# Performance work log

Hardware: AMD Instinct MI355X
Metric: run time of the kernel (lower is better)

## Reference

```python
import jax, jax.numpy as jnp
import numpy as np


def _up2(x):
    return jnp.repeat(jnp.repeat(x, 2, axis=2), 2, axis=3)


def setup_inputs() -> dict:
    key = jax.random.key(0)
    ks = jax.random.split(key, 6)
    Vps, C, H, W = 32, 128, 64, 64
    return {
        "x1": jax.random.normal(ks[0], (Vps, C, H, W), dtype=jnp.float32),
        "x2": jax.random.normal(ks[1], (Vps, C, H // 2, W // 2), dtype=jnp.float32),
        "x3": jax.random.normal(ks[2], (Vps, C, H // 4, W // 4), dtype=jnp.float32),
        "x4": jax.random.normal(ks[3], (Vps, C, H // 4, W // 4), dtype=jnp.float32),
        "conv_w": jax.random.normal(ks[4], (128, 512), dtype=jnp.float32) * 0.02,
        "conv_b": jnp.zeros((128,), dtype=jnp.float32),
        "gamma": jnp.zeros((1,), dtype=jnp.float32),
        "weight": jnp.ones((128,), dtype=jnp.float32),
        "lin_w": jax.random.normal(ks[5], (1, 128), dtype=jnp.float32) * 0.1,
    }


def reference(x1, x2, x3, x4, conv_w, conv_b, gamma, weight, lin_w):
    # upsample lower pyramid levels to x1 resolution and concat on channels
    x_sm = jnp.concatenate([x1, _up2(x2), _up2(_up2(x3)), _up2(_up2(x4))], axis=1)
    # 1x1 conv: [Vps,512,H,W] x [128,512] -> [Vps,128,H,W]
    x_sm = jnp.einsum('vchw,oc->vohw', x_sm, conv_w) + conv_b[None, :, None, None]
    Vps, C, H, W = x_sm.shape

    # --- batch (viewport) attention ---
    gap = jnp.mean(x_sm, axis=(2, 3))                     # [Vps, C]
    v_q = gap @ lin_w.T                                    # [Vps, 1]
    att = v_q @ v_q.T                                      # [Vps, Vps]
    att_new = jnp.broadcast_to(jnp.max(att, axis=-1, keepdims=True), att.shape)
    vps_mat = jax.nn.softmax(att_new, axis=-1)             # rows constant -> uniform
    v_v = x_sm.reshape(Vps, C * H * W)
    vps_att = (vps_mat @ v_v).reshape(Vps, C, H, W)
    x_sm = vps_att * gamma + x_sm

    # --- channel attention ---
    c_q = jnp.mean(x_sm, axis=(2, 3))                      # [Vps, C]
    att_C = c_q.T @ c_q                                    # [C, C]
    C_mat = jax.nn.softmax(att_C, axis=-1) * weight        # broadcast over last dim
    c_v = x_sm.reshape(C, Vps * H * W)                     # faithful raw reshape as in torch
    C_att = (C_mat @ c_v).reshape(Vps, C, H, W)
    out = C_att + x_sm
    return out.reshape(Vps, C, H * W)
```

## Files before the change

### kernel.cpp

```cpp
#include <hip/hip_runtime.h>

#define V 32
#define CH 128
#define SP 4096

typedef __attribute__((ext_vector_type(8))) short bf16x8;
typedef __attribute__((ext_vector_type(4))) float f32x4;

__device__ __forceinline__ unsigned short bf16rne(float x) {
    union { float f; unsigned u; } v; v.f = x;
    unsigned r = v.u + 0x7fff + ((v.u >> 16) & 1);
    return (unsigned short)(r >> 16);
}

__device__ __forceinline__ int xswz(int s) { return (s & 7) ^ ((s >> 2) & 7); }

__device__ __forceinline__ const float* xsm_row(const float* xsm, int j, int r) {
    return xsm + ((size_t)((j >> 2) * CH + (j & 3) * 32 + r)) * SP;
}

__global__ __launch_bounds__(128) void prep_w(const float* __restrict__ W,
                                              unsigned short* __restrict__ Wpad)
{
    int row = blockIdx.x;
    int j = threadIdx.x;
    int sigma = row >> 7, o = row & 127;
    Wpad[row * 128 + j] = bf16rne(W[o * 512 + sigma * 128 + j]);
}

__global__ __launch_bounds__(256) void conv_full(
    const float* __restrict__ x1, const float* __restrict__ x2,
    const float* __restrict__ x3, const float* __restrict__ x4,
    const unsigned short* __restrict__ Wpad, const float* __restrict__ bias,
    float* __restrict__ xsm, float* __restrict__ gap)
{
    __shared__ __align__(16) unsigned short Xl[64 * 128];
    __shared__ float gscr[4][64];
    const int v = blockIdx.y, sc = blockIdx.x, tid = threadIdx.x;
    const int lane = tid & 63, w = tid >> 6;
    const int l15 = lane & 15, quad = lane >> 4;
    const int o0 = (w >> 1) * 64, s0 = (w & 1) * 32;

    f32x4 acc[4][2];
#pragma unroll
    for (int it = 0; it < 4; ++it)
#pragma unroll
        for (int st = 0; st < 2; ++st) acc[it][st] = (f32x4){0.f, 0.f, 0.f, 0.f};

    auto mfma_chunk = [&](const unsigned short* __restrict__ Wsl) {
#pragma unroll
        for (int ks = 0; ks < 4; ++ks) {
            int kb = ks * 4 + quad;
            bf16x8 af[4], bfr[2];
#pragma unroll
            for (int it = 0; it < 4; ++it)
                af[it] = *(const bf16x8*)&Wsl[(o0 + it * 16 + l15) * 128 + ks * 32 + quad * 8];
#pragma unroll
            for (int st = 0; st < 2; ++st) {
                int s = s0 + st * 16 + l15;
                bfr[st] = *(const bf16x8*)&Xl[s * 128 + ((kb ^ xswz(s)) * 8)];
            }
#pragma unroll
            for (int it = 0; it < 4; ++it)
#pragma unroll
                for (int st = 0; st < 2; ++st)
                    acc[it][st] = __builtin_amdgcn_mfma_f32_16x16x32_bf16(
                        af[it], bfr[st], acc[it][st], 0, 0, 0);
        }
    };

    {
        const int sq = tid & 15, cp0 = tid >> 4;
        const float* xbase = x1 + (size_t)v * CH * SP + sc * 64;
#pragma unroll
        for (int rep = 0; rep < 4; ++rep) {
            int c = (cp0 + rep * 16) * 2;
            const float* r0 = xbase + (size_t)c * SP + sq * 4;
            float4 va = *(const float4*)r0;
            float4 vb = *(const float4*)(r0 + SP);
            float a4[4] = {va.x, va.y, va.z, va.w};
            float b4[4] = {vb.x, vb.y, vb.z, vb.w};
#pragma unroll
            for (int i = 0; i < 4; ++i) {
                int s = sq * 4 + i;
                ushort2 pk; pk.x = bf16rne(a4[i]); pk.y = bf16rne(b4[i]);
                *(ushort2*)&Xl[s * 128 + (((c >> 3) ^ xswz(s)) * 8) + (c & 7)] = pk;
            }
        }
    }
    __syncthreads();
    mfma_chunk(Wpad);
    __syncthreads();

    {
        const int sqq = tid & 3, c = (tid >> 2) * 2;
        const float* b2 = x2 + (size_t)(v * CH + c) * 1024 + (sc >> 1) * 32 + sqq * 8;
        float4 a0 = *(const float4*)b2;
        float4 a1 = *(const float4*)(b2 + 4);
        float4 b0 = *(const float4*)(b2 + 1024);
        float4 b1 = *(const float4*)(b2 + 1028);
        float av[8] = {a0.x, a0.y, a0.z, a0.w, a1.x, a1.y, a1.z, a1.w};
        float bv[8] = {b0.x, b0.y, b0.z, b0.w, b1.x, b1.y, b1.z, b1.w};
#pragma unroll
        for (int i = 0; i < 8; ++i) {
            ushort2 pk; pk.x = bf16rne(av[i]); pk.y = bf16rne(bv[i]);
            int w2 = sqq * 8 + i;
#pragma unroll
            for (int d = 0; d < 2; ++d) {
                int s = w2 * 2 + d;
                *(ushort2*)&Xl[s * 128 + (((c >> 3) ^ xswz(s)) * 8) + (c & 7)] = pk;
            }
        }
    }
    __syncthreads();
    mfma_chunk(Wpad + 1 * 128 * 128);
    __syncthreads();

#pragma unroll 1
    for (int ph = 0; ph < 2; ++ph) {
        const float* xp = ph ? x4 : x3;
        const int sqq = tid & 3, c = (tid >> 2) * 2;
        const float* b3 = xp + (size_t)(v * CH + c) * 256 + (sc >> 2) * 16 + sqq * 4;
        float4 a = *(const float4*)b3;
        float4 b = *(const float4*)(b3 + 256);
        float av[4] = {a.x, a.y, a.z, a.w};
        float bv[4] = {b.x, b.y, b.z, b.w};
#pragma unroll
        for (int i = 0; i < 4; ++i) {
            ushort2 pk; pk.x = bf16rne(av[i]); pk.y = bf16rne(bv[i]);
            int w4 = sqq * 4 + i;
#pragma unroll
            for (int d = 0; d < 4; ++d) {
                int s = w4 * 4 + d;
                *(ushort2*)&Xl[s * 128 + (((c >> 3) ^ xswz(s)) * 8) + (c & 7)] = pk;
            }
        }
        __syncthreads();
        mfma_chunk(Wpad + (2 + ph) * 128 * 128);
        __syncthreads();
    }

    float gs[16];
#pragma unroll
    for (int it = 0; it < 4; ++it)
#pragma unroll
        for (int reg = 0; reg < 4; ++reg) {
            int o = o0 + it * 16 + quad * 4 + reg;
            float b = bias[o];
            float* orow = xsm + ((size_t)(v * CH + o)) * SP + sc * 64;
            float lsum = 0.f;
#pragma unroll
            for (int st = 0; st < 2; ++st) {
                int s_l = s0 + st * 16 + l15;
                float val = acc[it][st][reg] + b;
                orow[s_l] = val;
                lsum += val;
            }
            gs[it * 4 + reg] = lsum;
        }
#pragma unroll
    for (int m = 1; m < 16; m <<= 1)
#pragma unroll
        for (int k = 0; k < 16; ++k) gs[k] += __shfl_xor(gs[k], m, 64);
    if (l15 == 0) {
#pragma unroll
        for (int it = 0; it < 4; ++it)
#pragma unroll
            for (int reg = 0; reg < 4; ++reg)
                gscr[w][it * 16 + quad * 4 + reg] = gs[it * 4 + reg];
    }
    __syncthreads();
    if (tid < 128) {
        int o = tid, b2i = (o >> 6) * 2;
        atomicAdd(&gap[v * CH + o], gscr[b2i][o & 63] + gscr[b2i + 1][o & 63]);
    }
}

__global__ __launch_bounds__(128) void build_G(
    const float* __restrict__ gap, const float* __restrict__ gammap,
    const float* __restrict__ weight, unsigned short* __restrict__ GsPad)
{
    __shared__ float cq[32][128];
    __shared__ float red[128];
    const int i = blockIdx.x, j = threadIdx.x;
    const float g = gammap[0];

    float gb = 0.f;
    for (int v = 0; v < 32; ++v) gb += gap[v * CH + j];
    gb = gb * (1.f / 32.f) * (1.f / 4096.f) * g;
    for (int v = 0; v < 32; ++v) cq[v][j] = gap[v * CH + j] * (1.f / 4096.f) + gb;
    __syncthreads();

    float a = 0.f;
    for (int v = 0; v < 32; ++v) a += cq[v][i] * cq[v][j];

    red[j] = a; __syncthreads();
    float m = -1e30f;
    for (int t = 0; t < 128; ++t) m = fmaxf(m, red[t]);
    __syncthreads();
    float e = __expf(a - m);
    red[j] = e; __syncthreads();
    float ssum = 0.f;
    for (int t = 0; t < 128; ++t) ssum += red[t];
    float cm = e / ssum * weight[j] + ((i == j) ? 1.f : 0.f);
    __syncthreads();
    red[j] = cm; __syncthreads();
    float rs = 0.f;
    for (int t = (j & 3); t < 128; t += 4) rs += red[t];
    float gfull = cm + g * (1.f / 32.f) * rs;
    GsPad[i * 128 + j] = bf16rne(gfull - ((i == j) ? 1.f : 0.f));
}

__global__ __launch_bounds__(256) void apply_G(
    float* __restrict__ xsm, const unsigned short* __restrict__ GsPad)
{
    __shared__ __align__(16) unsigned short Xl[64 * 128];
    const int r = blockIdx.y, sc = blockIdx.x, tid = threadIdx.x;
    const int lane = tid & 63, w = tid >> 6;
    const int l15 = lane & 15, quad = lane >> 4;
    const int i0 = (w >> 1) * 64, s0 = (w & 1) * 32;
    const int sq = tid & 15, cp0 = tid >> 4;

    f32x4 acc[4][2];
#pragma unroll
    for (int it = 0; it < 4; ++it)
#pragma unroll
        for (int st = 0; st < 2; ++st) acc[it][st] = (f32x4){0.f, 0.f, 0.f, 0.f};

#pragma unroll
    for (int rep = 0; rep < 4; ++rep) {
        int c = (cp0 + rep * 16) * 2;
        const float* r0 = xsm_row(xsm, c, r) + sc * 64 + sq * 4;
        const float* r1 = xsm_row(xsm, c + 1, r) + sc * 64 + sq * 4;
        float4 va = *(const float4*)r0;
        float4 vb = *(const float4*)r1;
        float a4[4] = {va.x, va.y, va.z, va.w};
        float b4[4] = {vb.x, vb.y, vb.z, vb.w};
#pragma unroll
        for (int i = 0; i < 4; ++i) {
            int s = sq * 4 + i;
            ushort2 pk; pk.x = bf16rne(a4[i]); pk.y = bf16rne(b4[i]);
            *(ushort2*)&Xl[s * 128 + (((c >> 3) ^ xswz(s)) * 8) + (c & 7)] = pk;
        }
    }
    __syncthreads();
#pragma unroll
    for (int ks = 0; ks < 4; ++ks) {
        int kb = ks * 4 + quad;
        bf16x8 af[4], bfr[2];
#pragma unroll
        for (int it = 0; it < 4; ++it)
            af[it] = *(const bf16x8*)&GsPad[(i0 + it * 16 + l15) * 128 + ks * 32 + quad * 8];
#pragma unroll
        for (int st = 0; st < 2; ++st) {
            int s = s0 + st * 16 + l15;
            bfr[st] = *(const bf16x8*)&Xl[s * 128 + ((kb ^ xswz(s)) * 8)];
        }
#pragma unroll
        for (int it = 0; it < 4; ++it)
#pragma unroll
            for (int st = 0; st < 2; ++st)
                acc[it][st] = __builtin_amdgcn_mfma_f32_16x16x32_bf16(
                    af[it], bfr[st], acc[it][st], 0, 0, 0);
    }
#pragma unroll
    for (int it = 0; it < 4; ++it)
#pragma unroll
        for (int reg = 0; reg < 4; ++reg) {
            int i = i0 + it * 16 + quad * 4 + reg;
            float* rowp = (float*)xsm_row(xsm, i, r) + sc * 64;
#pragma unroll
            for (int st = 0; st < 2; ++st) {
                int s_l = s0 + st * 16 + l15;
                rowp[s_l] = rowp[s_l] + acc[it][st][reg];
            }
        }
}

extern "C" void kernel_launch(void* const* d_in, const int* in_sizes, int n_in,
                              void* d_out, int out_size, void* d_ws, size_t ws_size,
                              hipStream_t stream)
{
    const float* x1     = (const float*)d_in[0];
    const float* x2     = (const float*)d_in[1];
    const float* x3     = (const float*)d_in[2];
    const float* x4     = (const float*)d_in[3];
    const float* conv_w = (const float*)d_in[4];
    const float* conv_b = (const float*)d_in[5];
    const float* gamma  = (const float*)d_in[6];
    const float* weight = (const float*)d_in[7];

    float* out = (float*)d_out;
    float* ws  = (float*)d_ws;

    float* gap = ws;
    unsigned short* Wpad  = (unsigned short*)(ws + 4096);
    unsigned short* GsPad = Wpad + 4 * 128 * 128;

    hipMemsetAsync(gap, 0, 4096 * sizeof(float), stream);

    prep_w<<<512, 128, 0, stream>>>(conv_w, Wpad);
    conv_full<<<dim3(64, 32), 256, 0, stream>>>(x1, x2, x3, x4, Wpad, conv_b, out, gap);
    build_G<<<128, 128, 0, stream>>>(gap, gamma, weight, GsPad);
    apply_G<<<dim3(64, 32), 256, 0, stream>>>(out, GsPad);
}
```

Before: 263.5 us.

## Stage swizzled weights in LDS and double spatial tile per block in conv and apply

Weight and G matrices are pre-laid-out in a swizzled bf16 image and copied into LDS, so MFMA operand A comes from shared memory instead of uncoalesced global loads. Each block now covers 128 spatial positions instead of 64, with the K dimension split into 64-wide chunks, which halves the grid and raises reuse of the weight operand. Accumulator count per thread doubles and LDS use grows, with launch bounds set to keep occupancy, at some cost in registers and extra synchronisation per chunk.

```diff
diff --git a/kernel.cpp b/kernel.cpp
--- a/kernel.cpp
+++ b/kernel.cpp
@@ -13,131 +13,134 @@
     return (unsigned short)(r >> 16);
 }
 
-__device__ __forceinline__ int xswz(int s) { return (s & 7) ^ ((s >> 2) & 7); }
-
-__device__ __forceinline__ const float* xsm_row(const float* xsm, int j, int r) {
+__device__ __forceinline__ int swz(int row) { return (row & 7) ^ ((row >> 2) & 7); }
+
+__device__ __forceinline__ float* xsm_row(float* xsm, int j, int r) {
     return xsm + ((size_t)((j >> 2) * CH + (j & 3) * 32 + r)) * SP;
 }
 
 __global__ __launch_bounds__(128) void prep_w(const float* __restrict__ W,
-                                              unsigned short* __restrict__ Wpad)
+                                              unsigned short* __restrict__ Wimg)
 {
     int row = blockIdx.x;
     int j = threadIdx.x;
     int sigma = row >> 7, o = row & 127;
-    Wpad[row * 128 + j] = bf16rne(W[o * 512 + sigma * 128 + j]);
-}
-
-__global__ __launch_bounds__(256) void conv_full(
+    int khalf = j >> 6, cl = j & 63;
+    int chunk = sigma * 2 + khalf;
+    int col = (((cl >> 3) ^ swz(o)) * 8) + (cl & 7);
+    Wimg[chunk * 8192 + o * 64 + col] = bf16rne(W[o * 512 + sigma * 128 + j]);
+}
+
+__global__ __launch_bounds__(256, 4) void conv_full(
     const float* __restrict__ x1, const float* __restrict__ x2,
     const float* __restrict__ x3, const float* __restrict__ x4,
-    const unsigned short* __restrict__ Wpad, const float* __restrict__ bias,
+    const unsigned short* __restrict__ Wimg, const float* __restrict__ bias,
     float* __restrict__ xsm, float* __restrict__ gap)
 {
-    __shared__ __align__(16) unsigned short Xl[64 * 128];
+    __shared__ __align__(16) unsigned short Wl[128 * 64];
+    __shared__ __align__(16) unsigned short Xl[128 * 64];
     __shared__ float gscr[4][64];
     const int v = blockIdx.y, sc = blockIdx.x, tid = threadIdx.x;
-    const int lane = tid & 63, w = tid >> 6;
+    const int lane = tid & 63, wv = tid >> 6;
     const int l15 = lane & 15, quad = lane >> 4;
-    const int o0 = (w >> 1) * 64, s0 = (w & 1) * 32;
-
-    f32x4 acc[4][2];
+    const int o0 = (wv >> 1) * 64, s0l = (wv & 1) * 64;
+
+    f32x4 acc[4][4];
 #pragma unroll
     for (int it = 0; it < 4; ++it)
 #pragma unroll
-        for (int st = 0; st < 2; ++st) acc[it][st] = (f32x4){0.f, 0.f, 0.f, 0.f};
-
-    auto mfma_chunk = [&](const unsigned short* __restrict__ Wsl) {
-#pragma unroll
-        for (int ks = 0; ks < 4; ++ks) {
+        for (int st = 0; st < 4; ++st) acc[it][st] = (f32x4){0.f, 0.f, 0.f, 0.f};
+
+#pragma unroll 1
+    for (int chunk = 0; chunk < 8; ++chunk) {
+        const int sigma = chunk >> 1, khalf = chunk & 1;
+        __syncthreads();
+        {
+            const float4* wsrc = (const float4*)(Wimg + chunk * 8192);
+            float4* wdst = (float4*)Wl;
+#pragma unroll
+            for (int p = 0; p < 4; ++p) wdst[tid + p * 256] = wsrc[tid + p * 256];
+        }
+        if (sigma == 0) {
+            int cp = tid >> 3, sq8 = tid & 7;
+            int c = cp * 2;
+            const float* xb = x1 + ((size_t)(v * CH + khalf * 64 + c)) * SP + sc * 128;
+#pragma unroll
+            for (int rep = 0; rep < 4; ++rep) {
+                int sq = sq8 + rep * 8;
+                float4 va = *(const float4*)(xb + sq * 4);
+                float4 vb = *(const float4*)(xb + SP + sq * 4);
+                float a4[4] = {va.x, va.y, va.z, va.w};
+                float b4[4] = {vb.x, vb.y, vb.z, vb.w};
+#pragma unroll
+                for (int i = 0; i < 4; ++i) {
+                    int s = sq * 4 + i;
+                    ushort2 pk; pk.x = bf16rne(a4[i]); pk.y = bf16rne(b4[i]);
+                    *(ushort2*)&Xl[s * 64 + (((c >> 3) ^ swz(s)) * 8) + (c & 7)] = pk;
+                }
+            }
+        } else if (sigma == 1) {
+            int cp = tid >> 3, wg = tid & 7;
+            int c = cp * 2;
+            const float* xb = x2 + ((size_t)(v * CH + khalf * 64 + c)) * 1024 + sc * 32 + wg * 4;
+            float4 va = *(const float4*)xb;
+            float4 vb = *(const float4*)(xb + 1024);
+            float a4[4] = {va.x, va.y, va.z, va.w};
+            float b4[4] = {vb.x, vb.y, vb.z, vb.w};
+#pragma unroll
+            for (int k = 0; k < 4; ++k) {
+                int w2 = wg * 4 + k;
+                ushort2 pk; pk.x = bf16rne(a4[k]); pk.y = bf16rne(b4[k]);
+#pragma unroll
+                for (int dh = 0; dh < 2; ++dh)
+#pragma unroll
+                    for (int dw = 0; dw < 2; ++dw) {
+                        int s = dh * 64 + w2 * 2 + dw;
+                        *(ushort2*)&Xl[s * 64 + (((c >> 3) ^ swz(s)) * 8) + (c & 7)] = pk;
+                    }
+            }
+        } else {
+            const float* xp = (sigma == 2) ? x3 : x4;
+            int cp = tid >> 3, sel = (tid >> 1) & 3, dh = tid & 1;
+            int c = cp * 2;
+            const float* xb = xp + ((size_t)(v * CH + khalf * 64 + c)) * 256 + (sc >> 1) * 16 + sel * 4;
+            float4 va = *(const float4*)xb;
+            float4 vb = *(const float4*)(xb + 256);
+            float a4[4] = {va.x, va.y, va.z, va.w};
+            float b4[4] = {vb.x, vb.y, vb.z, vb.w};
+#pragma unroll
+            for (int k = 0; k < 4; ++k) {
+                int w4 = sel * 4 + k;
+                ushort2 pk; pk.x = bf16rne(a4[k]); pk.y = bf16rne(b4[k]);
+#pragma unroll
+                for (int dw = 0; dw < 4; ++dw) {
+                    int s = dh * 64 + w4 * 4 + dw;
+                    *(ushort2*)&Xl[s * 64 + (((c >> 3) ^ swz(s)) * 8) + (c & 7)] = pk;
+                }
+            }
+        }
+        __syncthreads();
+#pragma unroll
+        for (int ks = 0; ks < 2; ++ks) {
             int kb = ks * 4 + quad;
-            bf16x8 af[4], bfr[2];
+            bf16x8 af[4], bfr[4];
+#pragma unroll
+            for (int it = 0; it < 4; ++it) {
+                int o = o0 + it * 16 + l15;
+                af[it] = *(const bf16x8*)&Wl[o * 64 + ((kb ^ swz(o)) * 8)];
+            }
+#pragma unroll
+            for (int st = 0; st < 4; ++st) {
+                int s = s0l + st * 16 + l15;
+                bfr[st] = *(const bf16x8*)&Xl[s * 64 + ((kb ^ swz(s)) * 8)];
+            }
 #pragma unroll
             for (int it = 0; it < 4; ++it)
-                af[it] = *(const bf16x8*)&Wsl[(o0 + it * 16 + l15) * 128 + ks * 32 + quad * 8];
-#pragma unroll
-            for (int st = 0; st < 2; ++st) {
-                int s = s0 + st * 16 + l15;
-                bfr[st] = *(const bf16x8*)&Xl[s * 128 + ((kb ^ xswz(s)) * 8)];
-            }
-#pragma unroll
-            for (int it = 0; it < 4; ++it)
-#pragma unroll
-                for (int st = 0; st < 2; ++st)
+#pragma unroll
+                for (int st = 0; st < 4; ++st)
                     acc[it][st] = __builtin_amdgcn_mfma_f32_16x16x32_bf16(
                         af[it], bfr[st], acc[it][st], 0, 0, 0);
         }
-    };
-
-    {
-        const int sq = tid & 15, cp0 = tid >> 4;
-        const float* xbase = x1 + (size_t)v * CH * SP + sc * 64;
-#pragma unroll
-        for (int rep = 0; rep < 4; ++rep) {
-            int c = (cp0 + rep * 16) * 2;
-            const float* r0 = xbase + (size_t)c * SP + sq * 4;
-            float4 va = *(const float4*)r0;
-            float4 vb = *(const float4*)(r0 + SP);
-            float a4[4] = {va.x, va.y, va.z, va.w};
-            float b4[4] = {vb.x, vb.y, vb.z, vb.w};
-#pragma unroll
-            for (int i = 0; i < 4; ++i) {
-                int s = sq * 4 + i;
-                ushort2 pk; pk.x = bf16rne(a4[i]); pk.y = bf16rne(b4[i]);
-                *(ushort2*)&Xl[s * 128 + (((c >> 3) ^ xswz(s)) * 8) + (c & 7)] = pk;
-            }
-        }
-    }
-    __syncthreads();
-    mfma_chunk(Wpad);
-    __syncthreads();
-
-    {
-        const int sqq = tid & 3, c = (tid >> 2) * 2;
-        const float* b2 = x2 + (size_t)(v * CH + c) * 1024 + (sc >> 1) * 32 + sqq * 8;
-        float4 a0 = *(const float4*)b2;
-        float4 a1 = *(const float4*)(b2 + 4);
-        float4 b0 = *(const float4*)(b2 + 1024);
-        float4 b1 = *(const float4*)(b2 + 1028);
-        float av[8] = {a0.x, a0.y, a0.z, a0.w, a1.x, a1.y, a1.z, a1.w};
-        float bv[8] = {b0.x, b0.y, b0.z, b0.w, b1.x, b1.y, b1.z, b1.w};
-#pragma unroll
-        for (int i = 0; i < 8; ++i) {
-            ushort2 pk; pk.x = bf16rne(av[i]); pk.y = bf16rne(bv[i]);
-            int w2 = sqq * 8 + i;
-#pragma unroll
-            for (int d = 0; d < 2; ++d) {
-                int s = w2 * 2 + d;
-                *(ushort2*)&Xl[s * 128 + (((c >> 3) ^ xswz(s)) * 8) + (c & 7)] = pk;
-            }
-        }
-    }
-    __syncthreads();
-    mfma_chunk(Wpad + 1 * 128 * 128);
-    __syncthreads();
-
-#pragma unroll 1
-    for (int ph = 0; ph < 2; ++ph) {
-        const float* xp = ph ? x4 : x3;
-        const int sqq = tid & 3, c = (tid >> 2) * 2;
-        const float* b3 = xp + (size_t)(v * CH + c) * 256 + (sc >> 2) * 16 + sqq * 4;
-        float4 a = *(const float4*)b3;
-        float4 b = *(const float4*)(b3 + 256);
-        float av[4] = {a.x, a.y, a.z, a.w};
-        float bv[4] = {b.x, b.y, b.z, b.w};
-#pragma unroll
-        for (int i = 0; i < 4; ++i) {
-            ushort2 pk; pk.x = bf16rne(av[i]); pk.y = bf16rne(bv[i]);
-            int w4 = sqq * 4 + i;
-#pragma unroll
-            for (int d = 0; d < 4; ++d) {
-                int s = w4 * 4 + d;
-                *(ushort2*)&Xl[s * 128 + (((c >> 3) ^ xswz(s)) * 8) + (c & 7)] = pk;
-            }
-        }
-        __syncthreads();
-        mfma_chunk(Wpad + (2 + ph) * 128 * 128);
-        __syncthreads();
     }
 
     float gs[16];
@@ -147,13 +150,13 @@
         for (int reg = 0; reg < 4; ++reg) {
             int o = o0 + it * 16 + quad * 4 + reg;
             float b = bias[o];
-            float* orow = xsm + ((size_t)(v * CH + o)) * SP + sc * 64;
+            float* orow = xsm + ((size_t)(v * CH + o)) * SP + sc * 128;
             float lsum = 0.f;
 #pragma unroll
-            for (int st = 0; st < 2; ++st) {
-                int s_l = s0 + st * 16 + l15;
+            for (int st = 0; st < 4; ++st) {
+                int sl = s0l + st * 16 + l15;
                 float val = acc[it][st][reg] + b;
-                orow[s_l] = val;
+                orow[sl] = val;
                 lsum += val;
             }
             gs[it * 4 + reg] = lsum;
@@ -167,18 +170,18 @@
         for (int it = 0; it < 4; ++it)
 #pragma unroll
             for (int reg = 0; reg < 4; ++reg)
-                gscr[w][it * 16 + quad * 4 + reg] = gs[it * 4 + reg];
+                gscr[wv][it * 16 + quad * 4 + reg] = gs[it * 4 + reg];
     }
     __syncthreads();
     if (tid < 128) {
-        int o = tid, b2i = (o >> 6) * 2;
-        atomicAdd(&gap[v * CH + o], gscr[b2i][o & 63] + gscr[b2i + 1][o & 63]);
+        int o = tid, b2 = (o >> 6) * 2;
+        atomicAdd(&gap[v * CH + o], gscr[b2][o & 63] + gscr[b2 + 1][o & 63]);
     }
 }
 
 __global__ __launch_bounds__(128) void build_G(
     const float* __restrict__ gap, const float* __restrict__ gammap,
-    const float* __restrict__ weight, unsigned short* __restrict__ GsPad)
+    const float* __restrict__ weight, unsigned short* __restrict__ Gimg)
 {
     __shared__ float cq[32][128];
     __shared__ float red[128];
@@ -208,71 +211,93 @@
     float rs = 0.f;
     for (int t = (j & 3); t < 128; t += 4) rs += red[t];
     float gfull = cm + g * (1.f / 32.f) * rs;
-    GsPad[i * 128 + j] = bf16rne(gfull - ((i == j) ? 1.f : 0.f));
-}
-
-__global__ __launch_bounds__(256) void apply_G(
-    float* __restrict__ xsm, const unsigned short* __restrict__ GsPad)
-{
-    __shared__ __align__(16) unsigned short Xl[64 * 128];
+    float gsv = gfull - ((i == j) ? 1.f : 0.f);
+    int jb = j >> 3;
+    int blk = (jb & 8) | ((jb & 7) ^ swz(i));
+    Gimg[i * 128 + blk * 8 + (j & 7)] = bf16rne(gsv);
+}
+
+__global__ __launch_bounds__(256, 3) void apply_G(
+    float* __restrict__ xsm, const unsigned short* __restrict__ Gimg)
+{
+    __shared__ __align__(16) unsigned short Gl[128 * 128];
+    __shared__ __align__(16) unsigned short Xl[128 * 64];
     const int r = blockIdx.y, sc = blockIdx.x, tid = threadIdx.x;
-    const int lane = tid & 63, w = tid >> 6;
+    const int lane = tid & 63, wv = tid >> 6;
     const int l15 = lane & 15, quad = lane >> 4;
-    const int i0 = (w >> 1) * 64, s0 = (w & 1) * 32;
-    const int sq = tid & 15, cp0 = tid >> 4;
-
-    f32x4 acc[4][2];
+    const int i0 = (wv >> 1) * 64, s0l = (wv & 1) * 64;
+
+    {
+        const float4* gsrc = (const float4*)Gimg;
+        float4* gdst = (float4*)Gl;
+#pragma unroll
+        for (int p = 0; p < 8; ++p) gdst[tid + p * 256] = gsrc[tid + p * 256];
+    }
+
+    f32x4 acc[4][4];
 #pragma unroll
     for (int it = 0; it < 4; ++it)
 #pragma unroll
-        for (int st = 0; st < 2; ++st) acc[it][st] = (f32x4){0.f, 0.f, 0.f, 0.f};
-
-#pragma unroll
-    for (int rep = 0; rep < 4; ++rep) {
-        int c = (cp0 + rep * 16) * 2;
-        const float* r0 = xsm_row(xsm, c, r) + sc * 64 + sq * 4;
-        const float* r1 = xsm_row(xsm, c + 1, r) + sc * 64 + sq * 4;
-        float4 va = *(const float4*)r0;
-        float4 vb = *(const float4*)r1;
-        float a4[4] = {va.x, va.y, va.z, va.w};
-        float b4[4] = {vb.x, vb.y, vb.z, vb.w};
-#pragma unroll
-        for (int i = 0; i < 4; ++i) {
-            int s = sq * 4 + i;
-            ushort2 pk; pk.x = bf16rne(a4[i]); pk.y = bf16rne(b4[i]);
-            *(ushort2*)&Xl[s * 128 + (((c >> 3) ^ xswz(s)) * 8) + (c & 7)] = pk;
-        }
-    }
-    __syncthreads();
-#pragma unroll
-    for (int ks = 0; ks < 4; ++ks) {
-        int kb = ks * 4 + quad;
-        bf16x8 af[4], bfr[2];
-#pragma unroll
-        for (int it = 0; it < 4; ++it)
-            af[it] = *(const bf16x8*)&GsPad[(i0 + it * 16 + l15) * 128 + ks * 32 + quad * 8];
-#pragma unroll
-        for (int st = 0; st < 2; ++st) {
-            int s = s0 + st * 16 + l15;
-            bfr[st] = *(const bf16x8*)&Xl[s * 128 + ((kb ^ xswz(s)) * 8)];
-        }
-#pragma unroll
-        for (int it = 0; it < 4; ++it)
-#pragma unroll
-            for (int st = 0; st < 2; ++st)
-                acc[it][st] = __builtin_amdgcn_mfma_f32_16x16x32_bf16(
-                    af[it], bfr[st], acc[it][st], 0, 0, 0);
+        for (int st = 0; st < 4; ++st) acc[it][st] = (f32x4){0.f, 0.f, 0.f, 0.f};
+
+#pragma unroll 1
+    for (int jc = 0; jc < 2; ++jc) {
+        __syncthreads();
+        {
+            int cp = tid >> 3, sq8 = tid & 7;
+            int c = cp * 2;
+            const float* ra = xsm_row(xsm, jc * 64 + c, r) + sc * 128;
+            const float* rb = xsm_row(xsm, jc * 64 + c + 1, r) + sc * 128;
+#pragma unroll
+            for (int rep = 0; rep < 4; ++rep) {
+                int sq = sq8 + rep * 8;
+                float4 va = *(const float4*)(ra + sq * 4);
+                float4 vb = *(const float4*)(rb + sq * 4);
+                float a4[4] = {va.x, va.y, va.z, va.w};
+                float b4[4] = {vb.x, vb.y, vb.z, vb.w};
+#pragma unroll
+                for (int i = 0; i < 4; ++i) {
+                    int s = sq * 4 + i;
+                    ushort2 pk; pk.x = bf16rne(a4[i]); pk.y = bf16rne(b4[i]);
+                    *(ushort2*)&Xl[s * 64 + (((c >> 3) ^ swz(s)) * 8) + (c & 7)] = pk;
+                }
+            }
+        }
+        __syncthreads();
+#pragma unroll
+        for (int ks = 0; ks < 2; ++ks) {
+            int kbl = ks * 4 + quad;
+            int kgl = jc * 8 + kbl;
+            bf16x8 af[4], bfr[4];
+#pragma unroll
+            for (int it = 0; it < 4; ++it) {
+                int i = i0 + it * 16 + l15;
+                int blk = (kgl & 8) | ((kgl & 7) ^ swz(i));
+                af[it] = *(const bf16x8*)&Gl[i * 128 + blk * 8];
+            }
+#pragma unroll
+            for (int st = 0; st < 4; ++st) {
+                int s = s0l + st * 16 + l15;
+                bfr[st] = *(const bf16x8*)&Xl[s * 64 + ((kbl ^ swz(s)) * 8)];
+            }
+#pragma unroll
+            for (int it = 0; it < 4; ++it)
+#pragma unroll
+                for (int st = 0; st < 4; ++st)
+                    acc[it][st] = __builtin_amdgcn_mfma_f32_16x16x32_bf16(
+                        af[it], bfr[st], acc[it][st], 0, 0, 0);
+        }
     }
 #pragma unroll
     for (int it = 0; it < 4; ++it)
 #pragma unroll
         for (int reg = 0; reg < 4; ++reg) {
             int i = i0 + it * 16 + quad * 4 + reg;
-            float* rowp = (float*)xsm_row(xsm, i, r) + sc * 64;
-#pragma unroll
-            for (int st = 0; st < 2; ++st) {
-                int s_l = s0 + st * 16 + l15;
-                rowp[s_l] = rowp[s_l] + acc[it][st][reg];
+            float* rowp = xsm_row(xsm, i, r) + sc * 128;
+#pragma unroll
+            for (int st = 0; st < 4; ++st) {
+                int sl = s0l + st * 16 + l15;
+                rowp[sl] = rowp[sl] + acc[it][st][reg];
             }
         }
 }
@@ -294,13 +319,13 @@
     float* ws  = (float*)d_ws;
 
     float* gap = ws;
-    unsigned short* Wpad  = (unsigned short*)(ws + 4096);
-    unsigned short* GsPad = Wpad + 4 * 128 * 128;
+    unsigned short* Wimg = (unsigned short*)(ws + 4096);
+    unsigned short* Gimg = Wimg + 8 * 8192;
 
     hipMemsetAsync(gap, 0, 4096 * sizeof(float), stream);
 
-    prep_w<<<512, 128, 0, stream>>>(conv_w, Wpad);
-    conv_full<<<dim3(64, 32), 256, 0, stream>>>(x1, x2, x3, x4, Wpad, conv_b, out, gap);
-    build_G<<<128, 128, 0, stream>>>(gap, gamma, weight, GsPad);
-    apply_G<<<dim3(64, 32), 256, 0, stream>>>(out, GsPad);
-}
+    prep_w<<<512, 128, 0, stream>>>(conv_w, Wimg);
+    conv_full<<<dim3(32, 32), 256, 0, stream>>>(x1, x2, x3, x4, Wimg, conv_b, out, gap);
+    build_G<<<128, 128, 0, stream>>>(gap, gamma, weight, Gimg);
+    apply_G<<<dim3(32, 32), 256, 0, stream>>>(out, Gimg);
+}
```

Measured after the change: 234.4 us. 1.12x faster.
